# Kernel optimization log

Measured on AMD Instinct MI355X. Metric: run time of the kernel, lower is better.

Reference implementation:

```python
import jax, jax.numpy as jnp
import numpy as np

B, T, D, H = 4, 2048, 1024, 16
HD = D // H  # head_dim = 64


def setup_inputs() -> dict:
    key = jax.random.key(0)
    k1, k2, k3 = jax.random.split(key, 3)
    scale_in = 1.0 / np.sqrt(D)
    return {
        "x": jax.random.normal(k1, (B, T, D), dtype=jnp.float32),
        "w_attn": jax.random.normal(k2, (D, 3 * D), dtype=jnp.float32) * scale_in,
        "b_attn": jnp.zeros((3 * D,), dtype=jnp.float32),
        "w_proj": jax.random.normal(k3, (D, D), dtype=jnp.float32) * scale_in,
        "b_proj": jnp.zeros((D,), dtype=jnp.float32),
    }


def reference(x, w_attn, b_attn, w_proj, b_proj):
    Bv, Tv, Dv = x.shape
    qkv = x @ w_attn + b_attn  # (B,T,3D)
    q, k, v = jnp.split(qkv, 3, axis=-1)
    # (B,T,D) -> (B,H,T,hd)
    q = q.reshape(Bv, Tv, H, HD).transpose(0, 2, 1, 3)
    k = k.reshape(Bv, Tv, H, HD).transpose(0, 2, 1, 3)
    v = v.reshape(Bv, Tv, H, HD).transpose(0, 2, 1, 3)
    scale = 1.0 / np.sqrt(HD)
    scores = jnp.einsum("bhqd,bhkd->bhqk", q, k) * scale  # (B,H,T,T)
    causal = jnp.tril(jnp.ones((Tv, Tv), dtype=bool))
    scores = jnp.where(causal, scores, jnp.finfo(scores.dtype).min)
    attn = jax.nn.softmax(scores, axis=-1)
    y = jnp.einsum("bhqk,bhkd->bhqd", attn, v)  # (B,H,T,hd)
    y = y.transpose(0, 2, 1, 3).reshape(Bv, Tv, Dv)
    return y @ w_proj + b_proj
```

## Files before the change

kernel.cpp:

```cpp
#include <hip/hip_runtime.h>
#include <math.h>

typedef __bf16 bf16_t;
typedef __attribute__((ext_vector_type(8))) __bf16 bf16x8;
typedef __attribute__((ext_vector_type(4))) float f32x4;

#define B_  4
#define T_  2048
#define D_  1024
#define H_  16
#define HD_ 64
#define D3_ 3072

__device__ __forceinline__ void load_lds16(const bf16_t* g, char* lds) {
  __builtin_amdgcn_global_load_lds(
      (const __attribute__((address_space(1))) void*)g,
      (__attribute__((address_space(3))) void*)lds, 16, 0, 0);
}

__global__ __launch_bounds__(256) void convert_bf16(
    const float* __restrict__ in, bf16_t* __restrict__ out, int n4) {
  int idx = blockIdx.x * 256 + threadIdx.x;
  int stride = gridDim.x * 256;
  for (int i = idx; i < n4; i += stride) {
    float4 v = ((const float4*)in)[i];
    alignas(8) bf16_t o4[4] = {(bf16_t)v.x, (bf16_t)v.y, (bf16_t)v.z, (bf16_t)v.w};
    ((uint2*)out)[i] = *(const uint2*)o4;
  }
}

__global__ __launch_bounds__(256) void transpose_convert(
    const float* __restrict__ W, bf16_t* __restrict__ Wt, int K, int N) {
  __shared__ float tile[64][65];
  const int k0 = blockIdx.x * 64, n0 = blockIdx.y * 64;
  const int tid = threadIdx.x;
  const int r = tid >> 4, c4 = (tid & 15) * 4;
#pragma unroll
  for (int i = 0; i < 4; ++i) {
    float4 v = *(const float4*)(W + (size_t)(k0 + r + i * 16) * N + n0 + c4);
    tile[r + i * 16][c4 + 0] = v.x;
    tile[r + i * 16][c4 + 1] = v.y;
    tile[r + i * 16][c4 + 2] = v.z;
    tile[r + i * 16][c4 + 3] = v.w;
  }
  __syncthreads();
#pragma unroll
  for (int i = 0; i < 4; ++i) {
    int n = r + i * 16;
    alignas(8) bf16_t o4[4];
#pragma unroll
    for (int j = 0; j < 4; ++j) o4[j] = (bf16_t)tile[c4 + j][n];
    *(uint2*)(Wt + (size_t)(n0 + n) * K + k0 + c4) = *(const uint2*)o4;
  }
}

#define GBM 128
#define GBN 128
#define GBK 32

template <bool BF16_OUT>
__global__ __launch_bounds__(256) void gemm_bt_mfma(
    const bf16_t* __restrict__ A, const bf16_t* __restrict__ Bt,
    const float* __restrict__ bias, void* __restrict__ Cv,
    int M, int N, int K) {
  __shared__ __align__(16) bf16_t Asl[2][GBM * GBK];
  __shared__ __align__(16) bf16_t Bsl[2][GBN * GBK];

  const int tid = threadIdx.x;
  const int w = tid >> 6, l = tid & 63;
  const int l15 = l & 15, lhi = l >> 4;
  const int row0 = blockIdx.y * GBM, col0 = blockIdx.x * GBN;
  const int wr = (w >> 1) * 64, wc = (w & 1) * 64;

  const int srow = tid >> 2;
  const int sf = (srow & 3) ^ ((srow >> 2) & 3);
  const int slog = (tid & 3) ^ sf;
  const int rf = (l15 & 3) ^ ((l15 >> 2) & 3);
  const int rchunk = lhi ^ rf;

  f32x4 acc[4][4];
#pragma unroll
  for (int i = 0; i < 4; ++i)
#pragma unroll
    for (int j = 0; j < 4; ++j) acc[i][j] = (f32x4){0.f, 0.f, 0.f, 0.f};

  const bf16_t* Abase = A + (size_t)row0 * K;
  const bf16_t* Bbase = Bt + (size_t)col0 * K;

  auto stage = [&](int buf, int k0) {
#pragma unroll
    for (int issue = 0; issue < 2; ++issue) {
      const bf16_t* ga = Abase + (size_t)(issue * 64 + srow) * K + k0 + slog * 8;
      load_lds16(ga, (char*)&Asl[buf][0] + issue * 4096 + w * 1024);
      const bf16_t* gb = Bbase + (size_t)(issue * 64 + srow) * K + k0 + slog * 8;
      load_lds16(gb, (char*)&Bsl[buf][0] + issue * 4096 + w * 1024);
    }
  };

  const int nt = K / GBK;
  stage(0, 0);

  for (int t = 0; t < nt; ++t) {
    __syncthreads();
    if (t + 1 < nt) stage((t + 1) & 1, (t + 1) * GBK);

    const bf16_t* As = &Asl[t & 1][0];
    const bf16_t* Bs = &Bsl[t & 1][0];
    bf16x8 af[4], bf[4];
#pragma unroll
    for (int i = 0; i < 4; ++i)
      af[i] = *(const bf16x8*)&As[(wr + i * 16 + l15) * GBK + rchunk * 8];
#pragma unroll
    for (int j = 0; j < 4; ++j)
      bf[j] = *(const bf16x8*)&Bs[(wc + j * 16 + l15) * GBK + rchunk * 8];
#pragma unroll
    for (int i = 0; i < 4; ++i)
#pragma unroll
      for (int j = 0; j < 4; ++j)
        acc[i][j] =
            __builtin_amdgcn_mfma_f32_16x16x32_bf16(af[i], bf[j], acc[i][j], 0, 0, 0);
  }

#pragma unroll
  for (int j = 0; j < 4; ++j) {
    int colr = col0 + wc + j * 16 + l15;
    float bv = bias[colr];
#pragma unroll
    for (int i = 0; i < 4; ++i) {
#pragma unroll
      for (int r = 0; r < 4; ++r) {
        int rowr = row0 + wr + i * 16 + lhi * 4 + r;
        float val = acc[i][j][r] + bv;
        if constexpr (BF16_OUT)
          ((bf16_t*)Cv)[(size_t)rowr * N + colr] = (bf16_t)val;
        else
          ((float*)Cv)[(size_t)rowr * N + colr] = val;
      }
    }
  }
}

__global__ __launch_bounds__(256) void transpose_v(
    const bf16_t* __restrict__ qkv, bf16_t* __restrict__ Vg) {
  const int bh = blockIdx.y;
  const int b = bh >> 4, h = bh & 15;
  const int t0 = blockIdx.x * 64;
  const int tid = threadIdx.x;
  const int d = tid & 63;
  const int w = tid >> 6;
  alignas(16) bf16_t tmp[16];
#pragma unroll
  for (int j = 0; j < 16; ++j) {
    int t = t0 + w * 16 + j;
    tmp[j] = qkv[(size_t)(b * T_ + t) * D3_ + 2 * D_ + h * HD_ + d];
  }
  bf16_t* dst = Vg + (size_t)(bh * HD_ + d) * T_ + t0 + w * 16;
  *(uint4*)(dst) = *(const uint4*)(tmp);
  *(uint4*)(dst + 8) = *(const uint4*)(tmp + 8);
}

#define QBLK 128
#define KBLK 64

__global__ __launch_bounds__(256, 4) void attn_fwd_mfma(
    const bf16_t* __restrict__ qkv, const bf16_t* __restrict__ Vg,
    bf16_t* __restrict__ y) {
  const int lin = blockIdx.x;
  const int bh = (lin & 7) * 8 + ((lin >> 3) & 7);
  const int qt = (T_ / QBLK - 1) - (lin >> 6);
  const int b = bh >> 4, h = bh & 15;
  const int Q0 = qt * QBLK;
  const int tid = threadIdx.x;
  const int w = tid >> 6, l = tid & 63;
  const int l15 = l & 15, lhi = l >> 4;

  __shared__ __align__(16) bf16_t K_lds[2][KBLK * 64];
  __shared__ __align__(16) bf16_t V_lds[KBLK * 64];
  __shared__ __align__(16) bf16_t P_lds[4][16][72];

  const int sr = tid >> 3, sp = tid & 7;
  const int slc = sp ^ (sr & 7);
  const int swz = (l15 & 7);

  auto stageK = [&](int buf, int kt) {
    const bf16_t* src =
        qkv + (size_t)(b * T_ + kt * KBLK + sr) * D3_ + D_ + h * HD_ + slc * 8;
    char* dst = (char*)(&K_lds[buf][0]) + w * 1024;
    load_lds16(src, dst);
    load_lds16(src + (size_t)32 * D3_, dst + 4096);
  };
  auto stageV = [&](int kt) {
    const bf16_t* src = Vg + ((size_t)bh * HD_ + sr) * T_ + kt * KBLK + slc * 8;
    char* dst = (char*)(&V_lds[0]) + w * 1024;
    load_lds16(src, dst);
    load_lds16(src + (size_t)32 * T_, dst + 4096);
  };

  bf16x8 qf[2][2];
#pragma unroll
  for (int g = 0; g < 2; ++g) {
    int q = Q0 + w * 32 + g * 16 + l15;
#pragma unroll
    for (int c = 0; c < 2; ++c) {
      const bf16_t* p = qkv + (size_t)(b * T_ + q) * D3_ + h * HD_ + c * 32 + lhi * 8;
      bf16x8 v = *(const bf16x8*)p;
#pragma unroll
      for (int e = 0; e < 8; ++e) v[e] = (bf16_t)((float)v[e] * 0.125f);
      qf[g][c] = v;
    }
  }

  f32x4 accO[2][4];
#pragma unroll
  for (int g = 0; g < 2; ++g)
#pragma unroll
    for (int dg = 0; dg < 4; ++dg) accO[g][dg] = (f32x4){0.f, 0.f, 0.f, 0.f};
  float m[2] = {-INFINITY, -INFINITY};
  float lsum[2] = {0.f, 0.f};

  const int ntiles = Q0 / KBLK + 2;
  const int qg0 = Q0 + w * 32;
  const int qg1 = qg0 + 16;

  stageK(0, 0);
  __syncthreads();

  for (int kt = 0; kt < ntiles; ++kt) {
    const int cur = kt & 1;
    const int ktb = kt * KBLK;
    stageV(kt);
    if (kt + 1 < ntiles) stageK(cur ^ 1, kt + 1);

    const bool act0 = (ktb <= qg0 + 15);
    const bool act1 = (ktb <= qg1 + 15);
    uint2 pp1[4];

#pragma unroll
    for (int g = 0; g < 2; ++g) {
      if (!(g == 0 ? act0 : act1)) continue;
      const int qg = g == 0 ? qg0 : qg1;

      f32x4 s[4];
#pragma unroll
      for (int n = 0; n < 4; ++n) s[n] = (f32x4){0.f, 0.f, 0.f, 0.f};
#pragma unroll
      for (int c = 0; c < 2; ++c) {
#pragma unroll
        for (int n = 0; n < 4; ++n) {
          bf16x8 kf = *(const bf16x8*)&K_lds[cur][(n * 16 + l15) * 64 +
                                                 (((c * 4 + lhi) ^ swz) * 8)];
          s[n] = __builtin_amdgcn_mfma_f32_16x16x32_bf16(kf, qf[g][c], s[n], 0, 0, 0);
        }
      }

      float sv[4][4];
#pragma unroll
      for (int n = 0; n < 4; ++n)
#pragma unroll
        for (int r = 0; r < 4; ++r) sv[n][r] = s[n][r];
      if (ktb + KBLK - 1 > qg) {
        const int qml = qg + l15 - ktb - lhi * 4;
#pragma unroll
        for (int n = 0; n < 4; ++n)
#pragma unroll
          for (int r = 0; r < 4; ++r)
            if (n * 16 + r > qml) sv[n][r] = -INFINITY;
      }

      float pm = sv[0][0];
#pragma unroll
      for (int n = 0; n < 4; ++n)
#pragma unroll
        for (int r = 0; r < 4; ++r) pm = fmaxf(pm, sv[n][r]);
      pm = fmaxf(pm, __shfl_xor(pm, 16));
      pm = fmaxf(pm, __shfl_xor(pm, 32));

      if (!__all(pm <= m[g] + 8.f)) {
        float mn = fmaxf(m[g], pm);
        float corrq = __expf(m[g] - mn);
        m[g] = mn;
        lsum[g] *= corrq;
        float cr[4];
#pragma unroll
        for (int r = 0; r < 4; ++r) cr[r] = __shfl(corrq, lhi * 4 + r);
#pragma unroll
        for (int dg = 0; dg < 4; ++dg)
#pragma unroll
          for (int r = 0; r < 4; ++r) accO[g][dg][r] *= cr[r];
      }
      const float mn = m[g];

      float rowsum = 0.f;
#pragma unroll
      for (int n = 0; n < 4; ++n) {
        alignas(8) bf16_t p4[4];
#pragma unroll
        for (int r = 0; r < 4; ++r) {
          float p = __expf(sv[n][r] - mn);
          rowsum += p;
          p4[r] = (bf16_t)p;
        }
        if (g == 0)
          *(uint2*)&P_lds[w][l15][n * 16 + lhi * 4] = *(const uint2*)p4;
        else
          pp1[n] = *(const uint2*)p4;
      }
      rowsum += __shfl_xor(rowsum, 16);
      rowsum += __shfl_xor(rowsum, 32);
      lsum[g] += rowsum;
    }

    __syncthreads();

    if (act0) {
#pragma unroll
      for (int c2 = 0; c2 < 2; ++c2) {
        bf16x8 pf = *(const bf16x8*)&P_lds[w][l15][c2 * 32 + lhi * 8];
#pragma unroll
        for (int dg = 0; dg < 4; ++dg) {
          bf16x8 vf = *(const bf16x8*)&V_lds[(dg * 16 + l15) * 64 +
                                             (((c2 * 4 + lhi) ^ swz) * 8)];
          accO[0][dg] =
              __builtin_amdgcn_mfma_f32_16x16x32_bf16(pf, vf, accO[0][dg], 0, 0, 0);
        }
      }
    }
    if (act1) {
#pragma unroll
      for (int n = 0; n < 4; ++n)
        *(uint2*)&P_lds[w][l15][n * 16 + lhi * 4] = pp1[n];
#pragma unroll
      for (int c2 = 0; c2 < 2; ++c2) {
        bf16x8 pf = *(const bf16x8*)&P_lds[w][l15][c2 * 32 + lhi * 8];
#pragma unroll
        for (int dg = 0; dg < 4; ++dg) {
          bf16x8 vf = *(const bf16x8*)&V_lds[(dg * 16 + l15) * 64 +
                                             (((c2 * 4 + lhi) ^ swz) * 8)];
          accO[1][dg] =
              __builtin_amdgcn_mfma_f32_16x16x32_bf16(pf, vf, accO[1][dg], 0, 0, 0);
        }
      }
    }

    __syncthreads();
  }

#pragma unroll
  for (int g = 0; g < 2; ++g)
#pragma unroll
    for (int r = 0; r < 4; ++r) {
      float ls = __shfl(lsum[g], lhi * 4 + r);
      float inv = 1.f / ls;
      int q = Q0 + w * 32 + g * 16 + lhi * 4 + r;
      bf16_t* yr = y + (size_t)(b * T_ + q) * D_ + h * HD_ + l15;
#pragma unroll
      for (int dg = 0; dg < 4; ++dg) yr[dg * 16] = (bf16_t)(accO[g][dg][r] * inv);
    }
}

extern "C" void kernel_launch(void* const* d_in, const int* in_sizes, int n_in,
                              void* d_out, int out_size, void* d_ws, size_t ws_size,
                              hipStream_t stream) {
  const float* x      = (const float*)d_in[0];
  const float* w_attn = (const float*)d_in[1];
  const float* b_attn = (const float*)d_in[2];
  const float* w_proj = (const float*)d_in[3];
  const float* b_proj = (const float*)d_in[4];
  float* out = (float*)d_out;

  const int M = B_ * T_;

  bf16_t* xb      = (bf16_t*)d_ws;
  bf16_t* wattnT  = xb + (size_t)M * D_;
  bf16_t* wprojT  = wattnT + (size_t)D3_ * D_;
  bf16_t* qkv_bf  = wprojT + (size_t)D_ * D_;
  bf16_t* Vg      = qkv_bf + (size_t)M * D3_;
  bf16_t* y_bf    = xb;

  convert_bf16<<<2048, 256, 0, stream>>>(x, xb, M * D_ / 4);
  transpose_convert<<<dim3(D_ / 64, D3_ / 64), 256, 0, stream>>>(w_attn, wattnT, D_, D3_);
  transpose_convert<<<dim3(D_ / 64, D_ / 64), 256, 0, stream>>>(w_proj, wprojT, D_, D_);
  gemm_bt_mfma<true><<<dim3(D3_ / GBN, M / GBM), 256, 0, stream>>>(
      xb, wattnT, b_attn, qkv_bf, M, D3_, D_);
  transpose_v<<<dim3(T_ / 64, B_ * H_), 256, 0, stream>>>(qkv_bf, Vg);
  attn_fwd_mfma<<<dim3(T_ / QBLK * B_ * H_), 256, 0, stream>>>(qkv_bf, Vg, y_bf);
  gemm_bt_mfma<false><<<dim3(D_ / GBN, M / GBM), 256, 0, stream>>>(
      y_bf, wprojT, b_proj, out, M, D_, D_);
}
```

Before: 190.3 us.

## Deepen attention K/V prefetch pipeline with triple-buffered K and double-buffered V

```diff
diff --git a/kernel.cpp b/kernel.cpp
--- a/kernel.cpp
+++ b/kernel.cpp
@@ -162,7 +162,7 @@
 #define QBLK 128
 #define KBLK 64
 
-__global__ __launch_bounds__(256, 4) void attn_fwd_mfma(
+__global__ __launch_bounds__(256, 3) void attn_fwd_mfma(
     const bf16_t* __restrict__ qkv, const bf16_t* __restrict__ Vg,
     bf16_t* __restrict__ y) {
   const int lin = blockIdx.x;
@@ -174,8 +174,8 @@
   const int w = tid >> 6, l = tid & 63;
   const int l15 = l & 15, lhi = l >> 4;
 
-  __shared__ __align__(16) bf16_t K_lds[2][KBLK * 64];
-  __shared__ __align__(16) bf16_t V_lds[KBLK * 64];
+  __shared__ __align__(16) bf16_t K_lds[3][KBLK * 64];
+  __shared__ __align__(16) bf16_t V_lds[2][KBLK * 64];
   __shared__ __align__(16) bf16_t P_lds[4][16][72];
 
   const int sr = tid >> 3, sp = tid & 7;
@@ -189,9 +189,9 @@
     load_lds16(src, dst);
     load_lds16(src + (size_t)32 * D3_, dst + 4096);
   };
-  auto stageV = [&](int kt) {
+  auto stageV = [&](int buf, int kt) {
     const bf16_t* src = Vg + ((size_t)bh * HD_ + sr) * T_ + kt * KBLK + slc * 8;
-    char* dst = (char*)(&V_lds[0]) + w * 1024;
+    char* dst = (char*)(&V_lds[buf][0]) + w * 1024;
     load_lds16(src, dst);
     load_lds16(src + (size_t)32 * T_, dst + 4096);
   };
@@ -209,6 +209,7 @@
       qf[g][c] = v;
     }
   }
+  asm volatile("s_waitcnt vmcnt(0)" ::: "memory");
 
   f32x4 accO[2][4];
 #pragma unroll
@@ -223,13 +224,21 @@
   const int qg1 = qg0 + 16;
 
   stageK(0, 0);
-  __syncthreads();
+  stageV(0, 0);
+  stageK(1, 1);
 
   for (int kt = 0; kt < ntiles; ++kt) {
-    const int cur = kt & 1;
+    asm volatile("s_waitcnt vmcnt(4)" ::: "memory");
+    __builtin_amdgcn_s_barrier();
+
+    const int vt = (kt + 1 < ntiles) ? kt + 1 : ntiles - 1;
+    const int kk = (kt + 2 < ntiles) ? kt + 2 : ntiles - 1;
+    stageV((kt + 1) & 1, vt);
+    stageK((kt + 2) % 3, kk);
+
+    const bf16_t* Kc = &K_lds[kt % 3][0];
+    const bf16_t* Vc = &V_lds[kt & 1][0];
     const int ktb = kt * KBLK;
-    stageV(kt);
-    if (kt + 1 < ntiles) stageK(cur ^ 1, kt + 1);
 
     const bool act0 = (ktb <= qg0 + 15);
     const bool act1 = (ktb <= qg1 + 15);
@@ -243,15 +252,17 @@
       f32x4 s[4];
 #pragma unroll
       for (int n = 0; n < 4; ++n) s[n] = (f32x4){0.f, 0.f, 0.f, 0.f};
+      __builtin_amdgcn_s_setprio(1);
 #pragma unroll
       for (int c = 0; c < 2; ++c) {
 #pragma unroll
         for (int n = 0; n < 4; ++n) {
-          bf16x8 kf = *(const bf16x8*)&K_lds[cur][(n * 16 + l15) * 64 +
-                                                 (((c * 4 + lhi) ^ swz) * 8)];
+          bf16x8 kf = *(const bf16x8*)&Kc[(n * 16 + l15) * 64 +
+                                          (((c * 4 + lhi) ^ swz) * 8)];
           s[n] = __builtin_amdgcn_mfma_f32_16x16x32_bf16(kf, qf[g][c], s[n], 0, 0, 0);
         }
       }
+      __builtin_amdgcn_s_setprio(0);
 
       float sv[4][4];
 #pragma unroll
@@ -310,39 +321,42 @@
       lsum[g] += rowsum;
     }
 
-    __syncthreads();
+    asm volatile("s_waitcnt vmcnt(6)" ::: "memory");
+    __builtin_amdgcn_s_barrier();
 
     if (act0) {
+      __builtin_amdgcn_s_setprio(1);
 #pragma unroll
       for (int c2 = 0; c2 < 2; ++c2) {
         bf16x8 pf = *(const bf16x8*)&P_lds[w][l15][c2 * 32 + lhi * 8];
 #pragma unroll
         for (int dg = 0; dg < 4; ++dg) {
-          bf16x8 vf = *(const bf16x8*)&V_lds[(dg * 16 + l15) * 64 +
-                                             (((c2 * 4 + lhi) ^ swz) * 8)];
+          bf16x8 vf = *(const bf16x8*)&Vc[(dg * 16 + l15) * 64 +
+                                          (((c2 * 4 + lhi) ^ swz) * 8)];
           accO[0][dg] =
               __builtin_amdgcn_mfma_f32_16x16x32_bf16(pf, vf, accO[0][dg], 0, 0, 0);
         }
       }
+      __builtin_amdgcn_s_setprio(0);
     }
     if (act1) {
 #pragma unroll
       for (int n = 0; n < 4; ++n)
         *(uint2*)&P_lds[w][l15][n * 16 + lhi * 4] = pp1[n];
+      __builtin_amdgcn_s_setprio(1);
 #pragma unroll
       for (int c2 = 0; c2 < 2; ++c2) {
         bf16x8 pf = *(const bf16x8*)&P_lds[w][l15][c2 * 32 + lhi * 8];
 #pragma unroll
         for (int dg = 0; dg < 4; ++dg) {
-          bf16x8 vf = *(const bf16x8*)&V_lds[(dg * 16 + l15) * 64 +
-                                             (((c2 * 4 + lhi) ^ swz) * 8)];
+          bf16x8 vf = *(const bf16x8*)&Vc[(dg * 16 + l15) * 64 +
+                                          (((c2 * 4 + lhi) ^ swz) * 8)];
           accO[1][dg] =
               __builtin_amdgcn_mfma_f32_16x16x32_bf16(pf, vf, accO[1][dg], 0, 0, 0);
         }
       }
-    }
-
-    __syncthreads();
+      __builtin_amdgcn_s_setprio(0);
+    }
   }
 
 #pragma unroll
```

Measured after the change: 196.8 us. 3.5% more time.

## Load K/V tiles directly into registers, drop shared-memory staging and block barriers

Applied to the files above, without the earlier changes.

```diff
diff --git a/kernel.cpp b/kernel.cpp
--- a/kernel.cpp
+++ b/kernel.cpp
@@ -162,39 +162,29 @@
 #define QBLK 128
 #define KBLK 64
 
-__global__ __launch_bounds__(256, 4) void attn_fwd_mfma(
+__global__ __launch_bounds__(256, 2) void attn_fwd_mfma(
     const bf16_t* __restrict__ qkv, const bf16_t* __restrict__ Vg,
     bf16_t* __restrict__ y) {
   const int lin = blockIdx.x;
-  const int bh = (lin & 7) * 8 + ((lin >> 3) & 7);
-  const int qt = (T_ / QBLK - 1) - (lin >> 6);
+  const int xcd = lin & 7, idx = lin >> 3;
+  const int bh = xcd * 8 + (idx & 7);
+  const int qt = (T_ / QBLK - 1) - (idx >> 3);
   const int b = bh >> 4, h = bh & 15;
   const int Q0 = qt * QBLK;
   const int tid = threadIdx.x;
   const int w = tid >> 6, l = tid & 63;
   const int l15 = l & 15, lhi = l >> 4;
 
-  __shared__ __align__(16) bf16_t K_lds[2][KBLK * 64];
-  __shared__ __align__(16) bf16_t V_lds[KBLK * 64];
-  __shared__ __align__(16) bf16_t P_lds[4][16][72];
-
-  const int sr = tid >> 3, sp = tid & 7;
-  const int slc = sp ^ (sr & 7);
-  const int swz = (l15 & 7);
-
-  auto stageK = [&](int buf, int kt) {
-    const bf16_t* src =
-        qkv + (size_t)(b * T_ + kt * KBLK + sr) * D3_ + D_ + h * HD_ + slc * 8;
-    char* dst = (char*)(&K_lds[buf][0]) + w * 1024;
-    load_lds16(src, dst);
-    load_lds16(src + (size_t)32 * D3_, dst + 4096);
-  };
-  auto stageV = [&](int kt) {
-    const bf16_t* src = Vg + ((size_t)bh * HD_ + sr) * T_ + kt * KBLK + slc * 8;
-    char* dst = (char*)(&V_lds[0]) + w * 1024;
-    load_lds16(src, dst);
-    load_lds16(src + (size_t)32 * T_, dst + 4096);
-  };
+  __shared__ __align__(16) bf16_t P_lds[4][2][16][72];
+
+  const bf16_t* kp[4];
+#pragma unroll
+  for (int n = 0; n < 4; ++n)
+    kp[n] = qkv + (size_t)(b * T_ + n * 16 + l15) * D3_ + D_ + h * HD_ + lhi * 8;
+  const bf16_t* vp[4];
+#pragma unroll
+  for (int dg = 0; dg < 4; ++dg)
+    vp[dg] = Vg + ((size_t)bh * HD_ + dg * 16 + l15) * T_ + lhi * 8;
 
   bf16x8 qf[2][2];
 #pragma unroll
@@ -222,18 +212,29 @@
   const int qg0 = Q0 + w * 32;
   const int qg1 = qg0 + 16;
 
-  stageK(0, 0);
-  __syncthreads();
-
-  for (int kt = 0; kt < ntiles; ++kt) {
-    const int cur = kt & 1;
+  bf16x8 KA[8], KB[8], VA[8];
+
+#define LOADK(DST, kt_)                                          \
+  {                                                              \
+    _Pragma("unroll") for (int n = 0; n < 4; ++n) {              \
+      const bf16_t* p_ = kp[n] + (size_t)(kt_) * (KBLK * D3_);   \
+      DST[n * 2 + 0] = *(const bf16x8*)(p_);                     \
+      DST[n * 2 + 1] = *(const bf16x8*)(p_ + 32);                \
+    }                                                            \
+  }
+#define LOADV(DST, kt_)                                          \
+  {                                                              \
+    _Pragma("unroll") for (int dg = 0; dg < 4; ++dg) {           \
+      const bf16_t* p_ = vp[dg] + (size_t)(kt_) * KBLK;          \
+      DST[dg * 2 + 0] = *(const bf16x8*)(p_);                    \
+      DST[dg * 2 + 1] = *(const bf16x8*)(p_ + 32);               \
+    }                                                            \
+  }
+
+  auto proc = [&](int kt, bf16x8(&Kc)[8], bf16x8(&Vc)[8]) {
     const int ktb = kt * KBLK;
-    stageV(kt);
-    if (kt + 1 < ntiles) stageK(cur ^ 1, kt + 1);
-
     const bool act0 = (ktb <= qg0 + 15);
     const bool act1 = (ktb <= qg1 + 15);
-    uint2 pp1[4];
 
 #pragma unroll
     for (int g = 0; g < 2; ++g) {
@@ -243,15 +244,14 @@
       f32x4 s[4];
 #pragma unroll
       for (int n = 0; n < 4; ++n) s[n] = (f32x4){0.f, 0.f, 0.f, 0.f};
-#pragma unroll
-      for (int c = 0; c < 2; ++c) {
-#pragma unroll
-        for (int n = 0; n < 4; ++n) {
-          bf16x8 kf = *(const bf16x8*)&K_lds[cur][(n * 16 + l15) * 64 +
-                                                 (((c * 4 + lhi) ^ swz) * 8)];
-          s[n] = __builtin_amdgcn_mfma_f32_16x16x32_bf16(kf, qf[g][c], s[n], 0, 0, 0);
-        }
-      }
+      __builtin_amdgcn_s_setprio(1);
+#pragma unroll
+      for (int c = 0; c < 2; ++c)
+#pragma unroll
+        for (int n = 0; n < 4; ++n)
+          s[n] = __builtin_amdgcn_mfma_f32_16x16x32_bf16(Kc[n * 2 + c], qf[g][c],
+                                                         s[n], 0, 0, 0);
+      __builtin_amdgcn_s_setprio(0);
 
       float sv[4][4];
 #pragma unroll
@@ -300,50 +300,51 @@
           rowsum += p;
           p4[r] = (bf16_t)p;
         }
-        if (g == 0)
-          *(uint2*)&P_lds[w][l15][n * 16 + lhi * 4] = *(const uint2*)p4;
-        else
-          pp1[n] = *(const uint2*)p4;
+        *(uint2*)&P_lds[w][g][l15][n * 16 + lhi * 4] = *(const uint2*)p4;
       }
       rowsum += __shfl_xor(rowsum, 16);
       rowsum += __shfl_xor(rowsum, 32);
       lsum[g] += rowsum;
     }
 
-    __syncthreads();
-
-    if (act0) {
+#pragma unroll
+    for (int g = 0; g < 2; ++g) {
+      if (!(g == 0 ? act0 : act1)) continue;
+      __builtin_amdgcn_s_setprio(1);
 #pragma unroll
       for (int c2 = 0; c2 < 2; ++c2) {
-        bf16x8 pf = *(const bf16x8*)&P_lds[w][l15][c2 * 32 + lhi * 8];
-#pragma unroll
-        for (int dg = 0; dg < 4; ++dg) {
-          bf16x8 vf = *(const bf16x8*)&V_lds[(dg * 16 + l15) * 64 +
-                                             (((c2 * 4 + lhi) ^ swz) * 8)];
-          accO[0][dg] =
-              __builtin_amdgcn_mfma_f32_16x16x32_bf16(pf, vf, accO[0][dg], 0, 0, 0);
-        }
-      }
-    }
-    if (act1) {
-#pragma unroll
-      for (int n = 0; n < 4; ++n)
-        *(uint2*)&P_lds[w][l15][n * 16 + lhi * 4] = pp1[n];
-#pragma unroll
-      for (int c2 = 0; c2 < 2; ++c2) {
-        bf16x8 pf = *(const bf16x8*)&P_lds[w][l15][c2 * 32 + lhi * 8];
-#pragma unroll
-        for (int dg = 0; dg < 4; ++dg) {
-          bf16x8 vf = *(const bf16x8*)&V_lds[(dg * 16 + l15) * 64 +
-                                             (((c2 * 4 + lhi) ^ swz) * 8)];
-          accO[1][dg] =
-              __builtin_amdgcn_mfma_f32_16x16x32_bf16(pf, vf, accO[1][dg], 0, 0, 0);
-        }
-      }
-    }
-
-    __syncthreads();
-  }
+        bf16x8 pf = *(const bf16x8*)&P_lds[w][g][l15][c2 * 32 + lhi * 8];
+#pragma unroll
+        for (int dg = 0; dg < 4; ++dg)
+          accO[g][dg] = __builtin_amdgcn_mfma_f32_16x16x32_bf16(
+              pf, Kc == KA ? Vc[dg * 2 + c2] : Vc[dg * 2 + c2], accO[g][dg], 0, 0, 0);
+      }
+      __builtin_amdgcn_s_setprio(0);
+    }
+  };
+
+  LOADK(KA, 0);
+  LOADV(VA, 0);
+
+  int kt = 0;
+  while (true) {
+    {
+      const int ktn = (kt + 1 < ntiles) ? kt + 1 : ntiles - 1;
+      LOADK(KB, ktn);
+      proc(kt, KA, VA);
+      if (++kt == ntiles) break;
+      LOADV(VA, kt);
+    }
+    {
+      const int ktn = (kt + 1 < ntiles) ? kt + 1 : ntiles - 1;
+      LOADK(KA, ktn);
+      proc(kt, KB, VA);
+      if (++kt == ntiles) break;
+      LOADV(VA, kt);
+    }
+  }
+#undef LOADK
+#undef LOADV
 
 #pragma unroll
   for (int g = 0; g < 2; ++g)
@@ -383,7 +384,7 @@
   gemm_bt_mfma<true><<<dim3(D3_ / GBN, M / GBM), 256, 0, stream>>>(
       xb, wattnT, b_attn, qkv_bf, M, D3_, D_);
   transpose_v<<<dim3(T_ / 64, B_ * H_), 256, 0, stream>>>(qkv_bf, Vg);
-  attn_fwd_mfma<<<dim3(T_ / QBLK * B_ * H_), 256, 0, stream>>>(qkv_bf, Vg, y_bf);
+  attn_fwd_mfma<<<1024, 256, 0, stream>>>(qkv_bf, Vg, y_bf);
   gemm_bt_mfma<false><<<dim3(D_ / GBN, M / GBM), 256, 0, stream>>>(
       y_bf, wprojT, b_proj, out, M, D_, D_);
 }
```

New measurement: 256.3 us. 1.35x slower.

## Double attention query tile to 256 rows with 8 waves and shared K reads

Applied to the files above, without the earlier changes.

```diff
diff --git a/kernel.cpp b/kernel.cpp
--- a/kernel.cpp
+++ b/kernel.cpp
@@ -159,15 +159,16 @@
   *(uint4*)(dst + 8) = *(const uint4*)(tmp + 8);
 }
 
-#define QBLK 128
+#define QBLK 256
 #define KBLK 64
 
-__global__ __launch_bounds__(256, 4) void attn_fwd_mfma(
+__global__ __launch_bounds__(512, 6) void attn_fwd_mfma(
     const bf16_t* __restrict__ qkv, const bf16_t* __restrict__ Vg,
     bf16_t* __restrict__ y) {
   const int lin = blockIdx.x;
-  const int bh = (lin & 7) * 8 + ((lin >> 3) & 7);
-  const int qt = (T_ / QBLK - 1) - (lin >> 6);
+  const int halfg = lin >> 8, idx = lin & 255;
+  const int bh = idx & 63;
+  const int qt = halfg ? (idx >> 6) : 7 - (idx >> 6);
   const int b = bh >> 4, h = bh & 15;
   const int Q0 = qt * QBLK;
   const int tid = threadIdx.x;
@@ -176,24 +177,20 @@
 
   __shared__ __align__(16) bf16_t K_lds[2][KBLK * 64];
   __shared__ __align__(16) bf16_t V_lds[KBLK * 64];
-  __shared__ __align__(16) bf16_t P_lds[4][16][72];
+  __shared__ __align__(16) bf16_t P_lds[8][16][72];
 
   const int sr = tid >> 3, sp = tid & 7;
   const int slc = sp ^ (sr & 7);
-  const int swz = (l15 & 7);
+  const int swz = l15 & 7;
 
   auto stageK = [&](int buf, int kt) {
     const bf16_t* src =
         qkv + (size_t)(b * T_ + kt * KBLK + sr) * D3_ + D_ + h * HD_ + slc * 8;
-    char* dst = (char*)(&K_lds[buf][0]) + w * 1024;
-    load_lds16(src, dst);
-    load_lds16(src + (size_t)32 * D3_, dst + 4096);
+    load_lds16(src, (char*)&K_lds[buf][0] + tid * 16);
   };
   auto stageV = [&](int kt) {
     const bf16_t* src = Vg + ((size_t)bh * HD_ + sr) * T_ + kt * KBLK + slc * 8;
-    char* dst = (char*)(&V_lds[0]) + w * 1024;
-    load_lds16(src, dst);
-    load_lds16(src + (size_t)32 * T_, dst + 4096);
+    load_lds16(src, (char*)&V_lds[0] + tid * 16);
   };
 
   bf16x8 qf[2][2];
@@ -218,7 +215,7 @@
   float m[2] = {-INFINITY, -INFINITY};
   float lsum[2] = {0.f, 0.f};
 
-  const int ntiles = Q0 / KBLK + 2;
+  const int ntiles = Q0 / KBLK + 4;
   const int qg0 = Q0 + w * 32;
   const int qg1 = qg0 + 16;
 
@@ -235,23 +232,33 @@
     const bool act1 = (ktb <= qg1 + 15);
     uint2 pp1[4];
 
+    f32x4 s0[4], s1[4];
+    if (act1) {
+#pragma unroll
+      for (int n = 0; n < 4; ++n) {
+        s0[n] = (f32x4){0.f, 0.f, 0.f, 0.f};
+        s1[n] = (f32x4){0.f, 0.f, 0.f, 0.f};
+      }
+      __builtin_amdgcn_s_setprio(1);
+#pragma unroll
+      for (int c = 0; c < 2; ++c) {
+#pragma unroll
+        for (int n = 0; n < 4; ++n) {
+          bf16x8 kf = *(const bf16x8*)&K_lds[cur][(n * 16 + l15) * 64 +
+                                                 (((c * 4 + lhi) ^ swz) * 8)];
+          if (act0)
+            s0[n] = __builtin_amdgcn_mfma_f32_16x16x32_bf16(kf, qf[0][c], s0[n], 0, 0, 0);
+          s1[n] = __builtin_amdgcn_mfma_f32_16x16x32_bf16(kf, qf[1][c], s1[n], 0, 0, 0);
+        }
+      }
+      __builtin_amdgcn_s_setprio(0);
+    }
+
 #pragma unroll
     for (int g = 0; g < 2; ++g) {
       if (!(g == 0 ? act0 : act1)) continue;
       const int qg = g == 0 ? qg0 : qg1;
-
-      f32x4 s[4];
-#pragma unroll
-      for (int n = 0; n < 4; ++n) s[n] = (f32x4){0.f, 0.f, 0.f, 0.f};
-#pragma unroll
-      for (int c = 0; c < 2; ++c) {
-#pragma unroll
-        for (int n = 0; n < 4; ++n) {
-          bf16x8 kf = *(const bf16x8*)&K_lds[cur][(n * 16 + l15) * 64 +
-                                                 (((c * 4 + lhi) ^ swz) * 8)];
-          s[n] = __builtin_amdgcn_mfma_f32_16x16x32_bf16(kf, qf[g][c], s[n], 0, 0, 0);
-        }
-      }
+      f32x4* s = g == 0 ? s0 : s1;
 
       float sv[4][4];
 #pragma unroll
@@ -313,6 +320,7 @@
     __syncthreads();
 
     if (act0) {
+      __builtin_amdgcn_s_setprio(1);
 #pragma unroll
       for (int c2 = 0; c2 < 2; ++c2) {
         bf16x8 pf = *(const bf16x8*)&P_lds[w][l15][c2 * 32 + lhi * 8];
@@ -324,11 +332,13 @@
               __builtin_amdgcn_mfma_f32_16x16x32_bf16(pf, vf, accO[0][dg], 0, 0, 0);
         }
       }
+      __builtin_amdgcn_s_setprio(0);
     }
     if (act1) {
 #pragma unroll
       for (int n = 0; n < 4; ++n)
         *(uint2*)&P_lds[w][l15][n * 16 + lhi * 4] = pp1[n];
+      __builtin_amdgcn_s_setprio(1);
 #pragma unroll
       for (int c2 = 0; c2 < 2; ++c2) {
         bf16x8 pf = *(const bf16x8*)&P_lds[w][l15][c2 * 32 + lhi * 8];
@@ -340,6 +350,7 @@
               __builtin_amdgcn_mfma_f32_16x16x32_bf16(pf, vf, accO[1][dg], 0, 0, 0);
         }
       }
+      __builtin_amdgcn_s_setprio(0);
     }
 
     __syncthreads();
@@ -383,7 +394,7 @@
   gemm_bt_mfma<true><<<dim3(D3_ / GBN, M / GBM), 256, 0, stream>>>(
       xb, wattnT, b_attn, qkv_bf, M, D3_, D_);
   transpose_v<<<dim3(T_ / 64, B_ * H_), 256, 0, stream>>>(qkv_bf, Vg);
-  attn_fwd_mfma<<<dim3(T_ / QBLK * B_ * H_), 256, 0, stream>>>(qkv_bf, Vg, y_bf);
+  attn_fwd_mfma<<<512, 512, 0, stream>>>(qkv_bf, Vg, y_bf);
   gemm_bt_mfma<false><<<dim3(D_ / GBN, M / GBM), 256, 0, stream>>>(
       y_bf, wprojT, b_proj, out, M, D_, D_);
 }
```

After: 540.4 us. +184.0%, slower.
